# Optimization experiments

Hardware: AMD Instinct MI355X
Metric: run time of the kernel (lower is better)

The kernel has to match this reference:

```python
import jax, jax.numpy as jnp
import numpy as np

L, S, N, E, H = 2048, 2048, 4, 1024, 16
D = E // H  # head_dim = 64


def setup_inputs() -> dict:
    key = jax.random.key(0)
    ks = jax.random.split(key, 7)
    scale = 1.0 / np.sqrt(E)
    return {
        "query": jax.random.normal(ks[0], (L, N, E), jnp.float32),
        "key": jax.random.normal(ks[1], (S, N, E), jnp.float32),
        "value": jax.random.normal(ks[2], (S, N, E), jnp.float32),
        "in_proj_w": jax.random.normal(ks[3], (3 * E, E), jnp.float32) * scale,
        "in_proj_b": jax.random.normal(ks[4], (3 * E,), jnp.float32) * 0.01,
        "out_proj_w": jax.random.normal(ks[5], (E, E), jnp.float32) * scale * 0.25,
        "out_proj_b": jax.random.normal(ks[6], (E,), jnp.float32) * 0.01,
    }


def reference(query, key, value, in_proj_w, in_proj_b, out_proj_w, out_proj_b):
    # Split packed in-projection into q/k/v parts (torch layout: [3E, E]).
    wq, wk, wv = in_proj_w[:E], in_proj_w[E:2 * E], in_proj_w[2 * E:]
    bq, bk, bv = in_proj_b[:E], in_proj_b[E:2 * E], in_proj_b[2 * E:]

    def proj(x, w, b):  # (T,N,E) -> (N,H,T,D)
        y = jnp.einsum('tne,fe->tnf', x, w) + b
        T = x.shape[0]
        return y.reshape(T, N, H, D).transpose(1, 2, 0, 3)

    q = proj(query, wq, bq) * (1.0 / np.sqrt(D))  # scale queries
    k = proj(key, wk, bk)
    v = proj(value, wv, bv)

    scores = jnp.einsum('nhld,nhsd->nhls', q, k)  # (N,H,L,S)
    attn = jax.nn.softmax(scores, axis=-1)
    ctx = jnp.einsum('nhls,nhsd->nhld', attn, v)  # (N,H,L,D)
    ctx = ctx.transpose(2, 0, 1, 3).reshape(L, N, E)  # (L,N,E)

    out = jnp.einsum('lne,fe->lnf', ctx, out_proj_w) + out_proj_b
    attn_weights = attn.mean(axis=1)  # (N,L,S), averaged over heads (torch default)
    return out, attn_weights
```

## Files before the change

kernel.cpp:

```cpp
#include <hip/hip_runtime.h>
#include <hip/hip_bf16.h>

#define L_ 2048
#define S_ 2048
#define NB 4
#define E_ 1024
#define H_ 16
#define D_ 64
#define LDT 72
#define NCH (S_ / 64)

typedef __attribute__((ext_vector_type(8))) short bf16x8;
typedef __attribute__((ext_vector_type(4))) float f32x4;

__device__ __forceinline__ short f2bf(float f) {
  union { float f; unsigned u; } v; v.f = f;
  unsigned r = v.u + 0x7FFFu + ((v.u >> 16) & 1u);
  return (short)(r >> 16);
}
__device__ __forceinline__ float bf2f(short s) {
  union { unsigned u; float f; } v; v.u = ((unsigned)(unsigned short)s) << 16;
  return v.f;
}
__device__ __forceinline__ unsigned cvt_pk_bf16(float lo, float hi) {
  unsigned r;
  asm("v_cvt_pk_bf16_f32 %0, %1, %2" : "=v"(r) : "v"(lo), "v"(hi));
  return r;
}

#define LGKM_BARRIER() do {                                   \
    asm volatile("s_waitcnt lgkmcnt(0)" ::: "memory");        \
    __builtin_amdgcn_sched_barrier(0);                        \
    __builtin_amdgcn_s_barrier();                             \
    __builtin_amdgcn_sched_barrier(0);                        \
  } while (0)

__global__ void k_convert(const float* __restrict__ wi, const float* __restrict__ wo,
                          short* __restrict__ wqkv, short* __restrict__ wout) {
  const int n1 = 3 * E_ * E_ / 4;
  const int n2 = E_ * E_ / 4;
  const int stride = gridDim.x * blockDim.x;
  for (int i = blockIdx.x * blockDim.x + threadIdx.x; i < n1 + n2; i += stride) {
    const float4* s; short* d; int j;
    if (i < n1) { s = (const float4*)wi; d = wqkv; j = i; }
    else        { s = (const float4*)wo; d = wout; j = i - n1; }
    float4 v = s[j];
    uint2 o; o.x = cvt_pk_bf16(v.x, v.y); o.y = cvt_pk_bf16(v.z, v.w);
    *(uint2*)&d[(size_t)j * 4] = o;
  }
}

__global__ __launch_bounds__(256) void k_qkv(
    const float* __restrict__ qin, const float* __restrict__ kin, const float* __restrict__ vin,
    const short* __restrict__ wbf, const float* __restrict__ bias,
    short* __restrict__ qh, short* __restrict__ kh, short* __restrict__ vh) {
  __shared__ short As[128 * LDT];
  __shared__ short Bs[128 * LDT];
  const int bm = blockIdx.x;
  const int fbase = blockIdx.y * 128;
  const int mat = fbase >> 10;
  const float* __restrict__ A = (mat == 0) ? qin : (mat == 1) ? kin : vin;
  short* __restrict__ dst = (mat == 0) ? qh : (mat == 1) ? kh : vh;
  const float scale = (mat == 0) ? 0.125f * 1.44269504088896f : 1.0f;
  const int tid = threadIdx.x;
  const int lane = tid & 63, wid = tid >> 6;
  const int wr = wid >> 1, wc = wid & 1;
  const int lr = lane & 15, lk = lane >> 4;
  f32x4 acc[4][4] = {};

  for (int kb = 0; kb < E_; kb += 64) {
#pragma unroll
    for (int i = 0; i < 8; ++i) {
      int f4 = i * 256 + tid;
      int row = f4 >> 4, k4 = f4 & 15;
      float4 v = *(const float4*)&A[(size_t)(bm * 128 + row) * E_ + kb + k4 * 4];
      uint2 o; o.x = cvt_pk_bf16(v.x, v.y); o.y = cvt_pk_bf16(v.z, v.w);
      *(uint2*)&As[row * LDT + k4 * 4] = o;
    }
#pragma unroll
    for (int i = 0; i < 4; ++i) {
      int e8 = i * 256 + tid;
      int row = e8 >> 3, k8 = e8 & 7;
      int4 v = *(const int4*)&wbf[(size_t)(fbase + row) * E_ + kb + k8 * 8];
      *(int4*)&Bs[row * LDT + k8 * 8] = v;
    }
    __syncthreads();
#pragma unroll
    for (int kk = 0; kk < 2; ++kk) {
      bf16x8 a[4], b[4];
#pragma unroll
      for (int fi = 0; fi < 4; ++fi)
        a[fi] = *(const bf16x8*)&As[(wr * 64 + fi * 16 + lr) * LDT + kk * 32 + lk * 8];
#pragma unroll
      for (int ci = 0; ci < 4; ++ci)
        b[ci] = *(const bf16x8*)&Bs[(wc * 64 + ci * 16 + lr) * LDT + kk * 32 + lk * 8];
#pragma unroll
      for (int fi = 0; fi < 4; ++fi)
#pragma unroll
        for (int ci = 0; ci < 4; ++ci)
          acc[fi][ci] = __builtin_amdgcn_mfma_f32_16x16x32_bf16(a[fi], b[ci], acc[fi][ci], 0, 0, 0);
    }
    __syncthreads();
  }
#pragma unroll
  for (int ci = 0; ci < 4; ++ci) {
    const int fg = fbase + wc * 64 + ci * 16 + lr;
    const float b = bias[fg];
    const int col = fg & 1023;
    const int h = col >> 6, d = col & 63;
#pragma unroll
    for (int fi = 0; fi < 4; ++fi)
#pragma unroll
      for (int j = 0; j < 4; ++j) {
        int m = bm * 128 + wr * 64 + fi * 16 + lk * 4 + j;
        int t = m >> 2, n = m & 3;
        float vv = (acc[fi][ci][j] + b) * scale;
        dst[(((size_t)(n * H_ + h) * L_ + t) << 6) + d] = f2bf(vv);
      }
  }
}

__global__ __launch_bounds__(256) void k_vtrans(const short* __restrict__ vh,
                                                short* __restrict__ vt) {
  __shared__ short t[64][LDT];
  const int nh = blockIdx.y;
  const int tb = blockIdx.x;
  const int tid = threadIdx.x;
  const short* __restrict__ src = vh + ((size_t)nh * L_ + tb * 64) * D_;
  short* __restrict__ dst = vt + (size_t)nh * S_ * D_;
#pragma unroll
  for (int i = 0; i < 2; ++i) {
    int v = i * 256 + tid;
    int r = v >> 3, c8 = v & 7;
    *(bf16x8*)&t[r][c8 * 8] = *(const bf16x8*)&src[(size_t)r * D_ + c8 * 8];
  }
  __syncthreads();
#pragma unroll
  for (int i = 0; i < 2; ++i) {
    int v = i * 256 + tid;
    int d = v >> 3, t8 = v & 7;
    bf16x8 o;
#pragma unroll
    for (int e = 0; e < 8; ++e) o[e] = t[t8 * 8 + e][d];
    int sb = tb * 2 + (t8 >> 2);
    *(bf16x8*)&dst[(size_t)sb * (D_ * 32) + d * 32 + (t8 & 3) * 8] = o;
  }
}

__global__ __launch_bounds__(256) void k_stats(
    const short* __restrict__ qh, const short* __restrict__ kh, float* __restrict__ rl) {
  const int nh = blockIdx.y;
  const int qt = blockIdx.x;
  const short* __restrict__ Q = qh + (size_t)nh * L_ * D_;
  const short* __restrict__ K = kh + (size_t)nh * S_ * D_;
  const int tid = threadIdx.x;
  const int lane = tid & 63, wid = tid >> 6;
  const int lr = lane & 15, lk = lane >> 4;
  const int rbase = qt * 128 + wid * 32;
  bf16x8 a[2][2];
#pragma unroll
  for (int ri = 0; ri < 2; ++ri)
#pragma unroll
    for (int kk = 0; kk < 2; ++kk)
      a[ri][kk] = *(const bf16x8*)&Q[(size_t)(rbase + ri * 16 + lr) * D_ + kk * 32 + lk * 8];
  bf16x8 kst[4][2];
#pragma unroll
  for (int ci = 0; ci < 4; ++ci) {
    kst[ci][0] = *(const bf16x8*)&K[(size_t)(ci * 16 + lr) * D_ + lk * 8];
    kst[ci][1] = *(const bf16x8*)&K[(size_t)(ci * 16 + lr) * D_ + 32 + lk * 8];
  }
  float ssum[2][4] = {};
  for (int st = 0; st < S_; st += 64) {
    const int stn = (st + 64 < S_) ? st + 64 : st;
    f32x4 acc[2][4] = {};
#pragma unroll
    for (int ci = 0; ci < 4; ++ci) {
#pragma unroll
      for (int ri = 0; ri < 2; ++ri) {
        acc[ri][ci] = __builtin_amdgcn_mfma_f32_16x16x32_bf16(a[ri][0], kst[ci][0], acc[ri][ci], 0, 0, 0);
        acc[ri][ci] = __builtin_amdgcn_mfma_f32_16x16x32_bf16(a[ri][1], kst[ci][1], acc[ri][ci], 0, 0, 0);
      }
      kst[ci][0] = *(const bf16x8*)&K[(size_t)(stn + ci * 16 + lr) * D_ + lk * 8];
      kst[ci][1] = *(const bf16x8*)&K[(size_t)(stn + ci * 16 + lr) * D_ + 32 + lk * 8];
    }
#pragma unroll
    for (int ri = 0; ri < 2; ++ri)
#pragma unroll
      for (int j = 0; j < 4; ++j) {
        float s = __builtin_amdgcn_exp2f(acc[ri][0][j]) + __builtin_amdgcn_exp2f(acc[ri][1][j]) +
                  __builtin_amdgcn_exp2f(acc[ri][2][j]) + __builtin_amdgcn_exp2f(acc[ri][3][j]);
        s += __shfl_xor(s, 1);
        s += __shfl_xor(s, 2);
        s += __shfl_xor(s, 4);
        s += __shfl_xor(s, 8);
        ssum[ri][j] += s;
      }
  }
  if (lr == 0) {
#pragma unroll
    for (int ri = 0; ri < 2; ++ri)
#pragma unroll
      for (int j = 0; j < 4; ++j)
        rl[(size_t)nh * L_ + rbase + ri * 16 + lk * 4 + j] = 1.0f / ssum[ri][j];
  }
}

__global__ __launch_bounds__(1024) void k_attn(
    const short* __restrict__ qh, const short* __restrict__ kh, const short* __restrict__ vt,
    const float* __restrict__ rl, float* __restrict__ attnw, short* __restrict__ ctx) {
  extern __shared__ char psl[];
  const int bid = blockIdx.x;
  const int xcd = bid & 7;
  const int n = xcd >> 1;
  const int qt = (bid >> 3) | ((xcd & 1) << 5);
  const int tid = threadIdx.x;
  const int h = tid >> 6, lane = tid & 63;
  const int lr = lane & 15, lk = lane >> 4;
  const int rbase = qt * 32;
  const size_t nh = (size_t)(n * H_ + h);
  const short* __restrict__ K = kh + nh * S_ * D_;
  const short* __restrict__ VT = vt + nh * S_ * D_;
  char* const slab0 = psl + h * 4096;

  bf16x8 qf[2][2];
  float rls[2];
  {
    const short* Q = qh + nh * L_ * D_;
#pragma unroll
    for (int li = 0; li < 2; ++li) {
#pragma unroll
      for (int kk = 0; kk < 2; ++kk)
        qf[li][kk] = *(const bf16x8*)&Q[(size_t)(rbase + li * 16 + lr) * D_ + kk * 32 + lk * 8];
      rls[li] = rl[nh * L_ + rbase + li * 16 + lr];
    }
  }
  f32x4 cacc[2][4] = {};
  const int mrow = tid >> 5, mc2 = (tid & 31) * 2;
  float* awp = attnw + ((size_t)n * L_ + rbase + mrow) * S_ + mc2;
  const int moff = mrow * 128 + ((mc2 * 2) ^ ((mrow & 7) << 4));

  for (int ch = 0; ch < NCH; ++ch) {
    const int st = ch * 64;
    char* const sl = slab0 + (ch & 1) * 65536;
    bf16x8 kf[4][2];
#pragma unroll
    for (int u = 0; u < 4; ++u) {
      kf[u][0] = *(const bf16x8*)&K[(size_t)(st + u * 16 + lr) * D_ + lk * 8];
      kf[u][1] = *(const bf16x8*)&K[(size_t)(st + u * 16 + lr) * D_ + 32 + lk * 8];
    }
    bf16x8 vb[4][2];
#pragma unroll
    for (int b = 0; b < 2; ++b) {
      const size_t sb = (size_t)((st >> 5) + b) * (D_ * 32);
#pragma unroll
      for (int ci = 0; ci < 4; ++ci)
        vb[ci][b] = *(const bf16x8*)&VT[sb + (ci * 16 + lr) * 32 + lk * 8];
    }
#pragma unroll
    for (int u = 0; u < 4; ++u) {
#pragma unroll
      for (int li = 0; li < 2; ++li) {
        f32x4 sc = {};
        sc = __builtin_amdgcn_mfma_f32_16x16x32_bf16(kf[u][0], qf[li][0], sc, 0, 0, 0);
        sc = __builtin_amdgcn_mfma_f32_16x16x32_bf16(kf[u][1], qf[li][1], sc, 0, 0, 0);
        uint2 pk;
        pk.x = cvt_pk_bf16(__builtin_amdgcn_exp2f(sc[0]) * rls[li],
                           __builtin_amdgcn_exp2f(sc[1]) * rls[li]);
        pk.y = cvt_pk_bf16(__builtin_amdgcn_exp2f(sc[2]) * rls[li],
                           __builtin_amdgcn_exp2f(sc[3]) * rls[li]);
        const int row = li * 16 + lr;
        *(uint2*)(sl + row * 128 + ((u * 32 + lk * 8) ^ ((row & 7) << 4))) = pk;
      }
    }
#pragma unroll
    for (int b = 0; b < 2; ++b)
#pragma unroll
      for (int li = 0; li < 2; ++li) {
        const int row = li * 16 + lr;
        bf16x8 pa = *(const bf16x8*)(sl + row * 128 + ((b * 64 + lk * 16) ^ ((row & 7) << 4)));
#pragma unroll
        for (int ci = 0; ci < 4; ++ci)
          cacc[li][ci] = __builtin_amdgcn_mfma_f32_16x16x32_bf16(pa, vb[ci][b], cacc[li][ci], 0, 0, 0);
      }
    if (ch > 0) {
      char* const ms = psl + (((ch & 1) ^ 1)) * 65536;
      float s0 = 0.f, s1 = 0.f;
#pragma unroll
      for (int hh = 0; hh < 16; ++hh) {
        short2 m = *(const short2*)(ms + hh * 4096 + moff);
        s0 += bf2f(m.x); s1 += bf2f(m.y);
      }
      *(float2*)&awp[st - 64] = make_float2(s0 * 0.0625f, s1 * 0.0625f);
    }
    LGKM_BARRIER();
  }
  {
    char* const ms = psl + 65536;
    float s0 = 0.f, s1 = 0.f;
#pragma unroll
    for (int hh = 0; hh < 16; ++hh) {
      short2 m = *(const short2*)(ms + hh * 4096 + moff);
      s0 += bf2f(m.x); s1 += bf2f(m.y);
    }
    *(float2*)&awp[S_ - 64] = make_float2(s0 * 0.0625f, s1 * 0.0625f);
  }
#pragma unroll
  for (int li = 0; li < 2; ++li)
#pragma unroll
    for (int ci = 0; ci < 4; ++ci)
#pragma unroll
      for (int j = 0; j < 4; ++j) {
        int row = rbase + li * 16 + lk * 4 + j;
        int d = ci * 16 + lr;
        ctx[((size_t)row * NB + n) * E_ + h * 64 + d] = f2bf(cacc[li][ci][j]);
      }
}

__global__ __launch_bounds__(256) void k_out(
    const short* __restrict__ ctxb, const short* __restrict__ wbf,
    const float* __restrict__ bias, float* __restrict__ out) {
  __shared__ short As[128 * LDT];
  __shared__ short Bs[128 * LDT];
  const int bm = blockIdx.x, bn = blockIdx.y;
  const int tid = threadIdx.x;
  const int lane = tid & 63, wid = tid >> 6;
  const int wr = wid >> 1, wc = wid & 1;
  const int lr = lane & 15, lk = lane >> 4;
  f32x4 acc[4][4] = {};
  for (int kb = 0; kb < E_; kb += 64) {
#pragma unroll
    for (int i = 0; i < 4; ++i) {
      int e8 = i * 256 + tid;
      int row = e8 >> 3, k8 = e8 & 7;
      int4 va = *(const int4*)&ctxb[(size_t)(bm * 128 + row) * E_ + kb + k8 * 8];
      *(int4*)&As[row * LDT + k8 * 8] = va;
      int4 vb = *(const int4*)&wbf[(size_t)(bn * 128 + row) * E_ + kb + k8 * 8];
      *(int4*)&Bs[row * LDT + k8 * 8] = vb;
    }
    __syncthreads();
#pragma unroll
    for (int kk = 0; kk < 2; ++kk) {
      bf16x8 a[4], b[4];
#pragma unroll
      for (int fi = 0; fi < 4; ++fi)
        a[fi] = *(const bf16x8*)&As[(wr * 64 + fi * 16 + lr) * LDT + kk * 32 + lk * 8];
#pragma unroll
      for (int ci = 0; ci < 4; ++ci)
        b[ci] = *(const bf16x8*)&Bs[(wc * 64 + ci * 16 + lr) * LDT + kk * 32 + lk * 8];
#pragma unroll
      for (int fi = 0; fi < 4; ++fi)
#pragma unroll
        for (int ci = 0; ci < 4; ++ci)
          acc[fi][ci] = __builtin_amdgcn_mfma_f32_16x16x32_bf16(a[fi], b[ci], acc[fi][ci], 0, 0, 0);
    }
    __syncthreads();
  }
#pragma unroll
  for (int ci = 0; ci < 4; ++ci) {
    int col = bn * 128 + wc * 64 + ci * 16 + lr;
    float b = bias[col];
#pragma unroll
    for (int fi = 0; fi < 4; ++fi)
#pragma unroll
      for (int j = 0; j < 4; ++j) {
        int m = bm * 128 + wr * 64 + fi * 16 + lk * 4 + j;
        out[(size_t)m * E_ + col] = acc[fi][ci][j] + b;
      }
  }
}

extern "C" void kernel_launch(void* const* d_in, const int* in_sizes, int n_in,
                              void* d_out, int out_size, void* d_ws, size_t ws_size,
                              hipStream_t stream) {
  const float* qin = (const float*)d_in[0];
  const float* kin = (const float*)d_in[1];
  const float* vin = (const float*)d_in[2];
  const float* wi  = (const float*)d_in[3];
  const float* bi  = (const float*)d_in[4];
  const float* wo  = (const float*)d_in[5];
  const float* bo  = (const float*)d_in[6];
  float* out = (float*)d_out;
  float* attnw = out + (size_t)L_ * NB * E_;

  short* wqkv = (short*)d_ws;
  short* wout = wqkv + (size_t)3 * E_ * E_;
  short* qh = wout + (size_t)E_ * E_;
  short* kh = qh + (size_t)NB * L_ * E_;
  short* vh = kh + (size_t)NB * L_ * E_;
  short* vt = vh + (size_t)NB * L_ * E_;
  float* rl = (float*)(vt + (size_t)NB * L_ * E_);
  short* ctx = (short*)(rl + (size_t)NB * H_ * L_);

  k_convert<<<1024, 256, 0, stream>>>(wi, wo, wqkv, wout);
  k_qkv<<<dim3(64, 24), 256, 0, stream>>>(qin, kin, vin, wqkv, bi, qh, kh, vh);
  k_vtrans<<<dim3(32, 64), 256, 0, stream>>>(vh, vt);
  k_stats<<<dim3(16, 64), 256, 0, stream>>>(qh, kh, rl);
  k_attn<<<256, 1024, 131072, stream>>>(qh, kh, vt, rl, attnw, ctx);
  k_out<<<dim3(64, 8), 256, 0, stream>>>(ctx, wout, bo, out);
}
```

Baseline: 453.0 us.

## Fuse V transpose into QKV epilogue, add MFMA priority, widen head-mean reduction

The QKV projection epilogue now writes V straight into the blocked transposed layout the attention kernel consumes, which removes the separate transpose kernel and its extra round trip through global memory. Inside the attention loop, MFMA sections are wrapped in s_setprio raises so matrix work gets issue priority. The head-averaged attention-weight reduction now has half the threads each read 4 bf16 values and write a float4, cutting instruction count. The V scatter stores in the QKV epilogue become strided two-byte writes, which may coalesce worse.

```diff
diff --git a/kernel.cpp b/kernel.cpp
--- a/kernel.cpp
+++ b/kernel.cpp
@@ -53,14 +53,14 @@
 __global__ __launch_bounds__(256) void k_qkv(
     const float* __restrict__ qin, const float* __restrict__ kin, const float* __restrict__ vin,
     const short* __restrict__ wbf, const float* __restrict__ bias,
-    short* __restrict__ qh, short* __restrict__ kh, short* __restrict__ vh) {
+    short* __restrict__ qh, short* __restrict__ kh, short* __restrict__ vt) {
   __shared__ short As[128 * LDT];
   __shared__ short Bs[128 * LDT];
   const int bm = blockIdx.x;
   const int fbase = blockIdx.y * 128;
   const int mat = fbase >> 10;
   const float* __restrict__ A = (mat == 0) ? qin : (mat == 1) ? kin : vin;
-  short* __restrict__ dst = (mat == 0) ? qh : (mat == 1) ? kh : vh;
+  short* __restrict__ dst = (mat == 0) ? qh : (mat == 1) ? kh : vt;
   const float scale = (mat == 0) ? 0.125f * 1.44269504088896f : 1.0f;
   const int tid = threadIdx.x;
   const int lane = tid & 63, wid = tid >> 6;
@@ -115,35 +115,12 @@
         int m = bm * 128 + wr * 64 + fi * 16 + lk * 4 + j;
         int t = m >> 2, n = m & 3;
         float vv = (acc[fi][ci][j] + b) * scale;
-        dst[(((size_t)(n * H_ + h) * L_ + t) << 6) + d] = f2bf(vv);
-      }
-  }
-}
-
-__global__ __launch_bounds__(256) void k_vtrans(const short* __restrict__ vh,
-                                                short* __restrict__ vt) {
-  __shared__ short t[64][LDT];
-  const int nh = blockIdx.y;
-  const int tb = blockIdx.x;
-  const int tid = threadIdx.x;
-  const short* __restrict__ src = vh + ((size_t)nh * L_ + tb * 64) * D_;
-  short* __restrict__ dst = vt + (size_t)nh * S_ * D_;
-#pragma unroll
-  for (int i = 0; i < 2; ++i) {
-    int v = i * 256 + tid;
-    int r = v >> 3, c8 = v & 7;
-    *(bf16x8*)&t[r][c8 * 8] = *(const bf16x8*)&src[(size_t)r * D_ + c8 * 8];
-  }
-  __syncthreads();
-#pragma unroll
-  for (int i = 0; i < 2; ++i) {
-    int v = i * 256 + tid;
-    int d = v >> 3, t8 = v & 7;
-    bf16x8 o;
-#pragma unroll
-    for (int e = 0; e < 8; ++e) o[e] = t[t8 * 8 + e][d];
-    int sb = tb * 2 + (t8 >> 2);
-    *(bf16x8*)&dst[(size_t)sb * (D_ * 32) + d * 32 + (t8 & 3) * 8] = o;
+        size_t base = (size_t)(n * H_ + h) * (L_ * D_);
+        size_t idx = (mat == 2)
+          ? base + (size_t)(t >> 5) * (D_ * 32) + d * 32 + (t & 31)
+          : base + ((size_t)t << 6) + d;
+        dst[idx] = f2bf(vv);
+      }
   }
 }
 
@@ -235,9 +212,9 @@
     }
   }
   f32x4 cacc[2][4] = {};
-  const int mrow = tid >> 5, mc2 = (tid & 31) * 2;
-  float* awp = attnw + ((size_t)n * L_ + rbase + mrow) * S_ + mc2;
-  const int moff = mrow * 128 + ((mc2 * 2) ^ ((mrow & 7) << 4));
+  const int mrow = tid >> 4, mc4 = (tid & 15) * 4;
+  float* awp = attnw + ((size_t)n * L_ + rbase + mrow) * S_ + mc4;
+  const int moff = mrow * 128 + ((mc4 * 2) ^ ((mrow & 7) << 4));
 
   for (int ch = 0; ch < NCH; ++ch) {
     const int st = ch * 64;
@@ -261,8 +238,10 @@
 #pragma unroll
       for (int li = 0; li < 2; ++li) {
         f32x4 sc = {};
+        __builtin_amdgcn_s_setprio(1);
         sc = __builtin_amdgcn_mfma_f32_16x16x32_bf16(kf[u][0], qf[li][0], sc, 0, 0, 0);
         sc = __builtin_amdgcn_mfma_f32_16x16x32_bf16(kf[u][1], qf[li][1], sc, 0, 0, 0);
+        __builtin_amdgcn_s_setprio(0);
         uint2 pk;
         pk.x = cvt_pk_bf16(__builtin_amdgcn_exp2f(sc[0]) * rls[li],
                            __builtin_amdgcn_exp2f(sc[1]) * rls[li]);
@@ -278,31 +257,37 @@
       for (int li = 0; li < 2; ++li) {
         const int row = li * 16 + lr;
         bf16x8 pa = *(const bf16x8*)(sl + row * 128 + ((b * 64 + lk * 16) ^ ((row & 7) << 4)));
+        __builtin_amdgcn_s_setprio(1);
 #pragma unroll
         for (int ci = 0; ci < 4; ++ci)
           cacc[li][ci] = __builtin_amdgcn_mfma_f32_16x16x32_bf16(pa, vb[ci][b], cacc[li][ci], 0, 0, 0);
-      }
-    if (ch > 0) {
+        __builtin_amdgcn_s_setprio(0);
+      }
+    if (ch > 0 && tid < 512) {
       char* const ms = psl + (((ch & 1) ^ 1)) * 65536;
-      float s0 = 0.f, s1 = 0.f;
+      float s0 = 0.f, s1 = 0.f, s2 = 0.f, s3 = 0.f;
 #pragma unroll
       for (int hh = 0; hh < 16; ++hh) {
-        short2 m = *(const short2*)(ms + hh * 4096 + moff);
-        s0 += bf2f(m.x); s1 += bf2f(m.y);
-      }
-      *(float2*)&awp[st - 64] = make_float2(s0 * 0.0625f, s1 * 0.0625f);
+        uint2 m = *(const uint2*)(ms + hh * 4096 + moff);
+        s0 += bf2f((short)(m.x & 0xFFFF)); s1 += bf2f((short)(m.x >> 16));
+        s2 += bf2f((short)(m.y & 0xFFFF)); s3 += bf2f((short)(m.y >> 16));
+      }
+      *(float4*)&awp[st - 64] = make_float4(s0 * 0.0625f, s1 * 0.0625f,
+                                            s2 * 0.0625f, s3 * 0.0625f);
     }
     LGKM_BARRIER();
   }
-  {
+  if (tid < 512) {
     char* const ms = psl + 65536;
-    float s0 = 0.f, s1 = 0.f;
+    float s0 = 0.f, s1 = 0.f, s2 = 0.f, s3 = 0.f;
 #pragma unroll
     for (int hh = 0; hh < 16; ++hh) {
-      short2 m = *(const short2*)(ms + hh * 4096 + moff);
-      s0 += bf2f(m.x); s1 += bf2f(m.y);
-    }
-    *(float2*)&awp[S_ - 64] = make_float2(s0 * 0.0625f, s1 * 0.0625f);
+      uint2 m = *(const uint2*)(ms + hh * 4096 + moff);
+      s0 += bf2f((short)(m.x & 0xFFFF)); s1 += bf2f((short)(m.x >> 16));
+      s2 += bf2f((short)(m.y & 0xFFFF)); s3 += bf2f((short)(m.y >> 16));
+    }
+    *(float4*)&awp[S_ - 64] = make_float4(s0 * 0.0625f, s1 * 0.0625f,
+                                          s2 * 0.0625f, s3 * 0.0625f);
   }
 #pragma unroll
   for (int li = 0; li < 2; ++li)
@@ -386,14 +371,12 @@
   short* wout = wqkv + (size_t)3 * E_ * E_;
   short* qh = wout + (size_t)E_ * E_;
   short* kh = qh + (size_t)NB * L_ * E_;
-  short* vh = kh + (size_t)NB * L_ * E_;
-  short* vt = vh + (size_t)NB * L_ * E_;
+  short* vt = kh + (size_t)NB * L_ * E_;
   float* rl = (float*)(vt + (size_t)NB * L_ * E_);
   short* ctx = (short*)(rl + (size_t)NB * H_ * L_);
 
   k_convert<<<1024, 256, 0, stream>>>(wi, wo, wqkv, wout);
-  k_qkv<<<dim3(64, 24), 256, 0, stream>>>(qin, kin, vin, wqkv, bi, qh, kh, vh);
-  k_vtrans<<<dim3(32, 64), 256, 0, stream>>>(vh, vt);
+  k_qkv<<<dim3(64, 24), 256, 0, stream>>>(qin, kin, vin, wqkv, bi, qh, kh, vt);
   k_stats<<<dim3(16, 64), 256, 0, stream>>>(qh, kh, rl);
   k_attn<<<256, 1024, 131072, stream>>>(qh, kh, vt, rl, attnw, ctx);
   k_out<<<dim3(64, 8), 256, 0, stream>>>(ctx, wout, bo, out);
```

New measurement: 495.5 us. 1.09x slower.
